# Performance work log

Measured on AMD Instinct MI355X. Metric: run time of the kernel, lower is better.

The kernel has to match this reference:

```python
import jax, jax.numpy as jnp
import numpy as np

D = 64
LENGTHS = (1, 32, 512)          # static BFS level sizes (traversal precomputed)
N_NODES = sum(LENGTHS)          # 545
BATCH = 2
NUM_PASSES = 2


def _lin_init(key, fan_in, fan_out):
    k1, k2 = jax.random.split(key)
    w = jax.random.normal(k1, (fan_out, fan_in), jnp.float32) / np.sqrt(fan_in)
    b = jax.random.normal(k2, (fan_out,), jnp.float32) * 0.01
    return w, b


def setup_inputs() -> dict:
    key = jax.random.key(0)
    ks = jax.random.split(key, 8)
    x = jax.random.normal(ks[0], (BATCH, N_NODES, D), jnp.float32)
    # tree edges consistent with LENGTHS (BFS levels, round-robin parent assignment)
    edges = []
    start_prev, start = 0, LENGTHS[0]
    for t, c in zip(LENGTHS, LENGTHS[1:]):
        for k in range(c):
            edges.append((start_prev + (k % t), start + k))
        start_prev = start
        start += c
    e = np.asarray(edges, dtype=np.int64).T  # [2, N-1]
    edge_index = jnp.broadcast_to(jnp.asarray(e)[None], (BATCH, 2, N_NODES - 1))
    w_ta, b_ta = _lin_init(ks[1], 2 * D, D)
    w_ca, b_ca = _lin_init(ks[2], 2 * D, D)
    w_tb, b_tb = _lin_init(ks[3], 2 * D, D)
    w_cb, b_cb = _lin_init(ks[4], 2 * D, D)
    w_u, b_u = _lin_init(ks[5], 2 * D, D)
    w_o, b_o = _lin_init(ks[6], 2 * D, D)
    w_mix = jax.random.normal(ks[7], (D, 1), jnp.float32)
    return {"x": x, "edge_index": edge_index,
            "w_ta": w_ta, "b_ta": b_ta, "w_ca": w_ca, "b_ca": b_ca,
            "w_tb": w_tb, "b_tb": b_tb, "w_cb": w_cb, "b_cb": b_cb,
            "w_mix": w_mix, "w_u": w_u, "b_u": b_u, "w_o": w_o, "b_o": b_o}


def reference(x, edge_index, w_ta, b_ta, w_ca, b_ca, w_tb, b_tb, w_cb, b_cb,
              w_mix, w_u, b_u, w_o, b_o):
    d = x.shape[-1]

    def gate_linear(w, b, main, s):
        # Linear(cat([main_col, s_k])) for every main column and every child k.
        # main: [d, m], s: [d, c] -> [c, d, m]
        return ((w[:, :d] @ main)[None, :, :]
                + (w[:, d:] @ s).T[:, :, None]
                + b[None, :, None])

    def prop(h, lengths):
        # h: [d, N]; update buffer accumulates across level pairs (as in source)
        update = jnp.zeros_like(h)
        offset = 0
        for t, c in zip(lengths, lengths[1:]):
            i, j = offset + t, offset + t + c
            T = h[:, offset:i]     # parent level  [d, t]
            C = h[:, i:j]          # child level   [d, c]
            Nb = h[:, offset:j]    # neighbors     [d, t+c]
            # softmax mix gate A, scaled by learned per-feature weight w_mix
            logits_a = jnp.concatenate(
                [gate_linear(w_ta, b_ta, T, C), gate_linear(w_ca, b_ca, C, C)], axis=-1)
            A = jax.nn.softmax(logits_a, axis=-1) * w_mix[None]   # [c, d, t+c]
            # softsign mix gate B
            pre_b = jnp.concatenate(
                [gate_linear(w_tb, b_tb, T, C), gate_linear(w_cb, b_cb, C, C)], axis=-1)
            Bm = pre_b / (1.0 + jnp.abs(pre_b))                   # [c, d, t+c]
            m = jnp.einsum('kdn,dn->kd', A + Bm, Nb)              # [c, d]
            s = C.T                                               # [c, d]
            u = jax.nn.sigmoid(m @ w_u[:, :d].T + s @ w_u[:, d:].T + b_u)
            o = jax.nn.relu(m @ w_o[:, :d].T + s @ w_o[:, d:].T + b_o)
            update = update.at[:, i:j].set((u * o + (1.0 - u) * m - s).T)
            h = h + update
            offset += t
        return h

    def per_graph(xg):  # xg: [N, d], already in BFS traversal order (perm = I)
        h = xg.T
        for _ in range(NUM_PASSES):
            h = prop(h, LENGTHS)
            h = prop(h, LENGTHS[::-1])
        return h.T

    return jax.vmap(per_graph)(x)
```

## Files before the change

### kernel.cpp

```cpp
#include <hip/hip_runtime.h>

#define D 64
#define NNODES 545
#define SNAPN 544
#define CN  64
#define CNP 32
#define NSL 4
#define NMS 8

__global__ void k_init(const float* __restrict__ x,
                       const float* __restrict__ w_ta, const float* __restrict__ w_ca,
                       const float* __restrict__ w_tb, const float* __restrict__ w_cb,
                       const float* __restrict__ w_u,  const float* __restrict__ w_o,
                       float* __restrict__ H, float* __restrict__ wT)
{
    int idx = blockIdx.x * 256 + threadIdx.x;
    const int NH = 2 * NNODES * D;
    if (idx < NH) { H[idx] = x[idx]; return; }
    int j = idx - NH;
    if (j >= 12 * 4096) return;
    int mat = j >> 12;
    int r   = j & 4095;
    int e   = r >> 6;
    int dd  = r & 63;
    const float* src;
    switch (mat >> 1) {
        case 0: src = w_ta; break;
        case 1: src = w_ca; break;
        case 2: src = w_tb; break;
        case 3: src = w_cb; break;
        case 4: src = w_u;  break;
        default: src = w_o; break;
    }
    int half = mat & 1;
    wT[j] = src[dd * 128 + half * 64 + e];
}

__global__ void k_stage(const float* __restrict__ H,
                        const float* __restrict__ wT,
                        float* __restrict__ snap,
                        float* __restrict__ Pb,
                        float* __restrict__ stT,
                        float* __restrict__ stC,
                        int off, int t, int c)
{
    __shared__ float Hs[4][64];
    __shared__ float PaS[4][64];
    int b = blockIdx.y;
    int tilesT = (t + 3) >> 2;
    int tile = blockIdx.x;
    int ln = threadIdx.x >> 6;
    int d  = threadIdx.x & 63;
    int regionC = (tile >= tilesT) ? 1 : 0;
    int tl = regionC ? (tile - tilesT) : tile;
    int n0 = tl * 4;
    int cnt = regionC ? c : t;
    int nodeBase = off + (regionC ? t : 0);
    int valid = (n0 + ln) < cnt;
    const float* Hb = H + b * NNODES * D;

    Hs[ln][d] = valid ? Hb[(nodeBase + n0 + ln) * D + d] : 0.0f;
    __syncthreads();

    const float* wA = wT + (regionC ? 2 * 4096 : 0);
    const float* wB = wT + (regionC ? 6 * 4096 : 4 * 4096);
    float acc_a = 0.0f, acc_b = 0.0f;
#pragma unroll 8
    for (int e = 0; e < 64; e++) {
        float h = Hs[ln][e];
        acc_a = fmaf(wA[e * 64 + d], h, acc_a);
        acc_b = fmaf(wB[e * 64 + d], h, acc_b);
    }
    int gn = (regionC ? t : 0) + n0 + ln;
    float* snapB = snap + b * SNAPN * D;
    float* PbB   = Pb   + b * SNAPN * D;
    if (valid) {
        PbB[gn * D + d]   = acc_b;
        snapB[gn * D + d] = Hs[ln][d];
    }
    PaS[ln][d] = valid ? acc_a : -3.0e38f;
    __syncthreads();

    if (threadIdx.x < 64) {
        int dd = threadIdx.x;
        float mx = -3.0e38f;
#pragma unroll
        for (int l = 0; l < 4; l++) mx = fmaxf(mx, PaS[l][dd]);
        int lim = cnt - n0; if (lim > 4) lim = 4;
        float se = 0.0f, sw = 0.0f;
        for (int l = 0; l < lim; l++) {
            float ev = expf(PaS[l][dd] - mx);
            se += ev;
            sw += ev * Hs[l][dd];
        }
        float* st = (regionC ? stC : stT) + b * 3 * 128 * 64;
        st[0 * 8192 + tl * 64 + dd] = mx;
        st[1 * 8192 + tl * 64 + dd] = se;
        st[2 * 8192 + tl * 64 + dd] = sw;
    }
}

__global__ void k_merge(const float* __restrict__ stT,
                        const float* __restrict__ stC,
                        float* __restrict__ stFin,
                        int t, int c)
{
    int r = blockIdx.x;
    int b = blockIdx.y;
    int d = threadIdx.x;
    const float* st = (r ? stC : stT) + b * 3 * 8192;
    int cnt = r ? c : t;
    int ntl = (cnt + 3) >> 2;
    float m = -3.0e38f, se = 0.0f, sw = 0.0f;
    for (int tl = 0; tl < ntl; tl++) {
        float m1 = st[tl * 64 + d];
        float s1 = st[8192 + tl * 64 + d];
        float w1 = st[2 * 8192 + tl * 64 + d];
        float nm = fmaxf(m, m1);
        float f0 = expf(m - nm), f1 = expf(m1 - nm);
        se = se * f0 + s1 * f1;
        sw = sw * f0 + w1 * f1;
        m  = nm;
    }
    float* o = stFin + (b * 2 + r) * 192;
    o[d] = m; o[64 + d] = se; o[128 + d] = sw;
}

__global__ void k_part(const float* __restrict__ wT,
                       const float* __restrict__ snap,
                       const float* __restrict__ Pb,
                       const float* __restrict__ b_tb, const float* __restrict__ b_cb,
                       const float* __restrict__ stT, const float* __restrict__ stC,
                       float* __restrict__ stMid,
                       float* __restrict__ accW,
                       int off, int t, int c)
{
    __shared__ float PS[CNP][D];
    __shared__ float SS[CNP][D];
    int kblk = gridDim.x - 4;
    int b  = blockIdx.z;

    if (blockIdx.x >= kblk) {
        if (threadIdx.x < 64) {
            int e = blockIdx.x - kblk;
            int r = e >> 1;
            int s = (e & 1) * 4 + blockIdx.y;
            int d = threadIdx.x;
            const float* st = (r ? stC : stT) + b * 3 * 8192;
            int cnt = r ? c : t;
            int ntl = (cnt + 3) >> 2;
            int tl0 = s * 16, tl1 = tl0 + 16; if (tl1 > ntl) tl1 = ntl;
            float m = -3.0e38f, se = 0.0f, sw = 0.0f;
            for (int tl = tl0; tl < tl1; tl++) {
                float m1 = st[tl * 64 + d];
                float s1 = st[8192 + tl * 64 + d];
                float w1 = st[2 * 8192 + tl * 64 + d];
                float nm = fmaxf(m, m1);
                float f0 = expf(m - nm), f1 = expf(m1 - nm);
                se = se * f0 + s1 * f1;
                sw = sw * f0 + w1 * f1;
                m  = nm;
            }
            float* o = stMid + ((b * 2 + r) * NMS + s) * 192;
            o[d] = m; o[64 + d] = se; o[128 + d] = sw;
        }
        return;
    }

    int s  = blockIdx.y;
    int kl = threadIdx.x >> 6;
    int d  = threadIdx.x & 63;
    int k  = blockIdx.x * 4 + kl;
    int valid = (k < c) ? 1 : 0;
    int kk = valid ? k : 0;
    const float* snapB = snap + b * SNAPN * D;
    const float* PbB   = Pb   + b * SNAPN * D;

    float offTb = b_tb[d], offCb = b_cb[d];
    const float* tbR = wT + 5 * 4096;
    const float* cbR = wT + 7 * 4096;
    const float* cptr = snapB + (t + kk) * 64;
#pragma unroll 8
    for (int e = 0; e < 64; e++) {
        float cv = cptr[e];
        offTb = fmaf(tbR[e * 64 + d], cv, offTb);
        offCb = fmaf(cbR[e * 64 + d], cv, offCb);
    }

    int NTOT = t + c;
    int nch = (NTOT + CNP - 1) / CNP;
    int cps = (nch + NSL - 1) / NSL;
    int ch0 = s * cps, ch1 = ch0 + cps; if (ch1 > nch) ch1 = nch;
    float acc = 0.0f;
    for (int ch = ch0; ch < ch1; ch++) {
        int n0 = ch * CNP;
        int cnt = NTOT - n0; if (cnt > CNP) cnt = CNP;
        __syncthreads();
        int tot4 = cnt * (D / 4);
        const float4* gp = (const float4*)(PbB   + n0 * D);
        const float4* gs = (const float4*)(snapB + n0 * D);
        float4* lp = (float4*)&PS[0][0];
        float4* ls = (float4*)&SS[0][0];
        for (int idx4 = threadIdx.x; idx4 < tot4; idx4 += 256) {
            lp[idx4] = gp[idx4];
            ls[idx4] = gs[idx4];
        }
        __syncthreads();
#pragma unroll 8
        for (int n = 0; n < cnt; n++) {
            int gn = n0 + n;
            float p = PS[n][d] + ((gn < t) ? offTb : offCb);
            float f = p / (1.0f + fabsf(p));
            acc = fmaf(f, SS[n][d], acc);
        }
    }
    accW[((s * 2 + b) * 512 + k) * 64 + d] = acc;
}

__global__ void k_fin(float* __restrict__ H,
                      const float* __restrict__ wT,
                      const float* __restrict__ snap,
                      const float* __restrict__ stMid,
                      const float* __restrict__ b_ta, const float* __restrict__ b_ca,
                      const float* __restrict__ w_mix,
                      const float* __restrict__ b_u, const float* __restrict__ b_o,
                      const float* __restrict__ accW,
                      float* __restrict__ updWS,
                      int off, int t, int c, int storeUpd, int reapply, int prev_i)
{
    __shared__ float mS[4][64];
    __shared__ float sS[4][64];
    int b  = blockIdx.y;
    int kl = threadIdx.x >> 6;
    int d  = threadIdx.x & 63;
    int k  = blockIdx.x * 4 + kl;
    int valid = (k < c) ? 1 : 0;
    int i = off + t;
    const float* snapB = snap + b * SNAPN * D;

    float mT = -3.0e38f, seT = 0.0f, swT = 0.0f;
    {
        const float* base = stMid + (b * 2 + 0) * NMS * 192;
#pragma unroll
        for (int s = 0; s < NMS; s++) {
            const float* p = base + s * 192;
            float m1 = p[d], s1 = p[64 + d], w1 = p[128 + d];
            float nm = fmaxf(mT, m1);
            float f0 = expf(mT - nm), f1 = expf(m1 - nm);
            seT = seT * f0 + s1 * f1;
            swT = swT * f0 + w1 * f1;
            mT = nm;
        }
    }
    float mC = -3.0e38f, seC = 0.0f, swC = 0.0f;
    {
        const float* base = stMid + (b * 2 + 1) * NMS * 192;
#pragma unroll
        for (int s = 0; s < NMS; s++) {
            const float* p = base + s * 192;
            float m1 = p[d], s1 = p[64 + d], w1 = p[128 + d];
            float nm = fmaxf(mC, m1);
            float f0 = expf(mC - nm), f1 = expf(m1 - nm);
            seC = seC * f0 + s1 * f1;
            swC = swC * f0 + w1 * f1;
            mC = nm;
        }
    }

    float offTa = b_ta[d], offCa = b_ca[d];
    const float* taR = wT + 1 * 4096;
    const float* caR = wT + 3 * 4096;
    int kk = valid ? k : 0;
    const float* cptr = snapB + (t + kk) * 64;
#pragma unroll 8
    for (int e = 0; e < 64; e++) {
        float cv = cptr[e];
        offTa = fmaf(taR[e * 64 + d], cv, offTa);
        offCa = fmaf(caR[e * 64 + d], cv, offCa);
    }

    float aT = mT + offTa, aC = mC + offCa;
    float M  = fmaxf(aT, aC);
    float eT = expf(aT - M), eC = expf(aC - M);
    float denom = eT * seT + eC * seC;
    float Apart = w_mix[d] * (eT * swT + eC * swC) / denom;

    float acc = 0.0f;
#pragma unroll
    for (int s = 0; s < NSL; s++) acc += accW[((s * 2 + b) * 512 + k) * 64 + d];
    float mval = Apart + acc;

    mS[kl][d] = mval;
    sS[kl][d] = snapB[(t + kk) * 64 + d];
    __syncthreads();

    const float* uL = wT + 8 * 4096;
    const float* uR = wT + 9 * 4096;
    const float* oL = wT + 10 * 4096;
    const float* oR = wT + 11 * 4096;
    float zU = b_u[d], zO = b_o[d];
#pragma unroll 8
    for (int e = 0; e < 64; e++) {
        float mv = mS[kl][e], sv = sS[kl][e];
        zU = fmaf(mv, uL[e * 64 + d], zU);
        zU = fmaf(sv, uR[e * 64 + d], zU);
        zO = fmaf(mv, oL[e * 64 + d], zO);
        zO = fmaf(sv, oR[e * 64 + d], zO);
    }
    float u  = 1.0f / (1.0f + expf(-zU));
    float o  = fmaxf(zO, 0.0f);
    float mm = mS[kl][d];
    float sv = sS[kl][d];
    float upd = u * o + (1.0f - u) * mm - sv;

    float* Hb = H + b * NNODES * D;
    if (valid) {
        Hb[(i + k) * D + d] += upd;
        if (storeUpd) updWS[b * 2048 + k * 64 + d] = upd;
    }
    if (reapply && blockIdx.x == 0) {
#pragma unroll
        for (int r = 0; r < 8; r++) {
            int idx = threadIdx.x + 256 * r;
            Hb[(prev_i + (idx >> 6)) * D + (idx & 63)] += updWS[b * 2048 + idx];
        }
    }
}

__global__ void k_gate(float* __restrict__ H,
                       const float* __restrict__ wT,
                       const float* __restrict__ snap,
                       const float* __restrict__ Pb,
                       const float* __restrict__ stFin,
                       const float* __restrict__ b_ta, const float* __restrict__ b_ca,
                       const float* __restrict__ b_tb, const float* __restrict__ b_cb,
                       const float* __restrict__ w_mix,
                       const float* __restrict__ b_u, const float* __restrict__ b_o,
                       float* __restrict__ updWS,
                       int off, int t, int c, int storeUpd, int reapply, int prev_i)
{
    __shared__ float PS[CN][D];
    __shared__ float SS[CN][D];
    __shared__ float mS[4][64];
    __shared__ float sS[4][64];
    int b  = blockIdx.y;
    int kl = threadIdx.x >> 6;
    int d  = threadIdx.x & 63;
    int k  = blockIdx.x * 4 + kl;
    int valid = (k < c) ? 1 : 0;
    int i = off + t;
    const float* snapB = snap + b * SNAPN * D;
    const float* PbB   = Pb   + b * SNAPN * D;

    const float* fB = stFin + b * 384;
    float mT = fB[d],       seT = fB[64 + d],  swT = fB[128 + d];
    float mC = fB[192 + d], seC = fB[256 + d], swC = fB[320 + d];

    float offTa = b_ta[d], offCa = b_ca[d], offTb = b_tb[d], offCb = b_cb[d];
    const float* taR = wT + 1 * 4096;
    const float* caR = wT + 3 * 4096;
    const float* tbR = wT + 5 * 4096;
    const float* cbR = wT + 7 * 4096;
    int kk = valid ? k : 0;
    const float* cptr = snapB + (t + kk) * 64;
#pragma unroll 8
    for (int e = 0; e < 64; e++) {
        float cv = cptr[e];
        offTa = fmaf(taR[e * 64 + d], cv, offTa);
        offCa = fmaf(caR[e * 64 + d], cv, offCa);
        offTb = fmaf(tbR[e * 64 + d], cv, offTb);
        offCb = fmaf(cbR[e * 64 + d], cv, offCb);
    }

    float aT = mT + offTa, aC = mC + offCa;
    float M  = fmaxf(aT, aC);
    float eT = expf(aT - M), eC = expf(aC - M);
    float denom = eT * seT + eC * seC;
    float Apart = w_mix[d] * (eT * swT + eC * swC) / denom;

    float acc = 0.0f;
    int NTOT = t + c;
    for (int n0 = 0; n0 < NTOT; n0 += CN) {
        int cnt = NTOT - n0; if (cnt > CN) cnt = CN;
        __syncthreads();
        int tot4 = cnt * (D / 4);
        const float4* gp = (const float4*)(PbB   + n0 * D);
        const float4* gs = (const float4*)(snapB + n0 * D);
        float4* lp = (float4*)&PS[0][0];
        float4* ls = (float4*)&SS[0][0];
        for (int idx4 = threadIdx.x; idx4 < tot4; idx4 += 256) {
            lp[idx4] = gp[idx4];
            ls[idx4] = gs[idx4];
        }
        __syncthreads();
#pragma unroll 8
        for (int n = 0; n < cnt; n++) {
            int gn = n0 + n;
            float p = PS[n][d] + ((gn < t) ? offTb : offCb);
            float f = p / (1.0f + fabsf(p));
            acc = fmaf(f, SS[n][d], acc);
        }
    }
    float mval = Apart + acc;

    mS[kl][d] = mval;
    sS[kl][d] = snapB[(t + kk) * 64 + d];
    __syncthreads();

    const float* uL = wT + 8 * 4096;
    const float* uR = wT + 9 * 4096;
    const float* oL = wT + 10 * 4096;
    const float* oR = wT + 11 * 4096;
    float zU = b_u[d], zO = b_o[d];
#pragma unroll 8
    for (int e = 0; e < 64; e++) {
        float mv = mS[kl][e], sv = sS[kl][e];
        zU = fmaf(mv, uL[e * 64 + d], zU);
        zU = fmaf(sv, uR[e * 64 + d], zU);
        zO = fmaf(mv, oL[e * 64 + d], zO);
        zO = fmaf(sv, oR[e * 64 + d], zO);
    }
    float u  = 1.0f / (1.0f + expf(-zU));
    float o  = fmaxf(zO, 0.0f);
    float mm = mS[kl][d];
    float sv = sS[kl][d];
    float upd = u * o + (1.0f - u) * mm - sv;

    float* Hb = H + b * NNODES * D;
    if (valid) {
        Hb[(i + k) * D + d] += upd;
        if (storeUpd) updWS[b * 2048 + k * 64 + d] = upd;
    }
    if (reapply && blockIdx.x == 0) {
#pragma unroll
        for (int r = 0; r < 8; r++) {
            int idx = threadIdx.x + 256 * r;
            Hb[(prev_i + (idx >> 6)) * D + (idx & 63)] += updWS[b * 2048 + idx];
        }
    }
}

extern "C" void kernel_launch(void* const* d_in, const int* in_sizes, int n_in,
                              void* d_out, int out_size, void* d_ws, size_t ws_size,
                              hipStream_t stream) {
    const float* x    = (const float*)d_in[0];
    const float* w_ta = (const float*)d_in[2];
    const float* b_ta = (const float*)d_in[3];
    const float* w_ca = (const float*)d_in[4];
    const float* b_ca = (const float*)d_in[5];
    const float* w_tb = (const float*)d_in[6];
    const float* b_tb = (const float*)d_in[7];
    const float* w_cb = (const float*)d_in[8];
    const float* b_cb = (const float*)d_in[9];
    const float* w_mix= (const float*)d_in[10];
    const float* w_u  = (const float*)d_in[11];
    const float* b_u  = (const float*)d_in[12];
    const float* w_o  = (const float*)d_in[13];
    const float* b_o  = (const float*)d_in[14];

    float* H  = (float*)d_out;
    float* ws = (float*)d_ws;
    float* wT    = ws;
    float* snap  = wT + 49152;
    float* Pb    = snap + 69632;
    float* stT   = Pb + 69632;
    float* stC   = stT + 49152;
    float* upd   = stC + 49152;
    float* stFin = upd + 4096;
    float* accW  = stFin + 768;
    float* stMid = accW + 262144;

    const size_t NEEDED = (size_t)(49152 + 69632 + 69632 + 49152 + 49152 + 4096 + 768
                                   + (size_t)NSL * 2 * 512 * 64 + 2 * 2 * NMS * 192) * 4;
    int useSplit = (ws_size >= NEEDED) ? 1 : 0;

    {
        int total = 2 * NNODES * D + 12 * 4096;
        k_init<<<dim3((total + 255) / 256), 256, 0, stream>>>(
            x, w_ta, w_ca, w_tb, w_cb, w_u, w_o, H, wT);
    }

    struct St { int off, t, c, store, reapply, prev_i; };
    const St steps[4] = {
        {0,   1,  32, 1, 0, 0},
        {1,  32, 512, 0, 1, 1},
        {0, 512,  32, 1, 0, 0},
        {512, 32,  1, 0, 1, 512},
    };
    for (int p = 0; p < 2; p++) {
        for (int s = 0; s < 4; s++) {
            St st = steps[s];
            int tilesT = (st.t + 3) / 4, tilesC = (st.c + 3) / 4;
            k_stage<<<dim3(tilesT + tilesC, 2), 256, 0, stream>>>(
                H, wT, snap, Pb, stT, stC, st.off, st.t, st.c);
            int kblk = (st.c + 3) / 4;
            if (useSplit) {
                k_part<<<dim3(kblk + 4, NSL, 2), 256, 0, stream>>>(
                    wT, snap, Pb, b_tb, b_cb, stT, stC, stMid, accW,
                    st.off, st.t, st.c);
                k_fin<<<dim3(kblk, 2), 256, 0, stream>>>(
                    H, wT, snap, stMid, b_ta, b_ca, w_mix, b_u, b_o, accW, upd,
                    st.off, st.t, st.c, st.store, st.reapply, st.prev_i);
            } else {
                k_merge<<<dim3(2, 2), 64, 0, stream>>>(
                    stT, stC, stFin, st.t, st.c);
                k_gate<<<dim3(kblk, 2), 256, 0, stream>>>(
                    H, wT, snap, Pb, stFin,
                    b_ta, b_ca, b_tb, b_cb, w_mix, b_u, b_o, upd,
                    st.off, st.t, st.c, st.store, st.reapply, st.prev_i);
            }
        }
    }
}
```

Measured before the change: 220.7 us.

## Fuse tiny-level gate steps into one kernel and widen split-K for large levels

Adds a fused k_gate4 kernel for levels where t+c <= 64. It merges the softmax stats, gate offsets, the softsign accumulation and the update in one launch, removing the separate k_part/k_fin launches for those steps. For the larger levels the split count rises from 4 to 8, and the k_part inner loop reads Pb/snap straight from global memory instead of staging through shared memory with barriers. This trades launch count and barrier overhead for more partial-sum traffic in accW and uncached global reads.

```diff
diff --git a/kernel.cpp b/kernel.cpp
--- a/kernel.cpp
+++ b/kernel.cpp
@@ -5,7 +5,7 @@
 #define SNAPN 544
 #define CN  64
 #define CNP 32
-#define NSL 4
+#define NSLMAX 16
 #define NMS 8
 
 __global__ void k_init(const float* __restrict__ x,
@@ -126,6 +126,141 @@
     o[d] = m; o[64 + d] = se; o[128 + d] = sw;
 }
 
+__global__ void k_gate4(float* __restrict__ H,
+                        const float* __restrict__ wT,
+                        const float* __restrict__ snap,
+                        const float* __restrict__ Pb,
+                        const float* __restrict__ stT,
+                        const float* __restrict__ stC,
+                        const float* __restrict__ b_ta, const float* __restrict__ b_ca,
+                        const float* __restrict__ b_tb, const float* __restrict__ b_cb,
+                        const float* __restrict__ w_mix,
+                        const float* __restrict__ b_u, const float* __restrict__ b_o,
+                        float* __restrict__ updWS,
+                        int off, int t, int c, int storeUpd, int reapply, int prev_i)
+{
+    __shared__ float PS[CN][D];
+    __shared__ float SS[CN][D];
+    __shared__ float mS[4][64];
+    __shared__ float sS[4][64];
+    int b  = blockIdx.y;
+    int kl = threadIdx.x >> 6;
+    int d  = threadIdx.x & 63;
+    int k  = blockIdx.x * 4 + kl;
+    int valid = (k < c) ? 1 : 0;
+    int i = off + t;
+    const float* snapB = snap + b * SNAPN * D;
+    const float* PbB   = Pb   + b * SNAPN * D;
+
+    int nT = (t + 3) >> 2, nC = (c + 3) >> 2;
+    const float* sT = stT + b * 3 * 8192;
+    float mT = -3.0e38f, seT = 0.0f, swT = 0.0f;
+    for (int tl = 0; tl < nT; tl++) {
+        float m1 = sT[tl * 64 + d];
+        float s1 = sT[8192 + tl * 64 + d];
+        float w1 = sT[2 * 8192 + tl * 64 + d];
+        float nm = fmaxf(mT, m1);
+        float f0 = expf(mT - nm), f1 = expf(m1 - nm);
+        seT = seT * f0 + s1 * f1;
+        swT = swT * f0 + w1 * f1;
+        mT = nm;
+    }
+    const float* sC = stC + b * 3 * 8192;
+    float mC = -3.0e38f, seC = 0.0f, swC = 0.0f;
+    for (int tl = 0; tl < nC; tl++) {
+        float m1 = sC[tl * 64 + d];
+        float s1 = sC[8192 + tl * 64 + d];
+        float w1 = sC[2 * 8192 + tl * 64 + d];
+        float nm = fmaxf(mC, m1);
+        float f0 = expf(mC - nm), f1 = expf(m1 - nm);
+        seC = seC * f0 + s1 * f1;
+        swC = swC * f0 + w1 * f1;
+        mC = nm;
+    }
+
+    float offTa = b_ta[d], offCa = b_ca[d], offTb = b_tb[d], offCb = b_cb[d];
+    const float* taR = wT + 1 * 4096;
+    const float* caR = wT + 3 * 4096;
+    const float* tbR = wT + 5 * 4096;
+    const float* cbR = wT + 7 * 4096;
+    int kk = valid ? k : 0;
+    const float* cptr = snapB + (t + kk) * 64;
+#pragma unroll 4
+    for (int e = 0; e < 64; e++) {
+        float cv = cptr[e];
+        offTa = fmaf(taR[e * 64 + d], cv, offTa);
+        offCa = fmaf(caR[e * 64 + d], cv, offCa);
+        offTb = fmaf(tbR[e * 64 + d], cv, offTb);
+        offCb = fmaf(cbR[e * 64 + d], cv, offCb);
+    }
+
+    float aT = mT + offTa, aC = mC + offCa;
+    float M  = fmaxf(aT, aC);
+    float eT = expf(aT - M), eC = expf(aC - M);
+    float denom = eT * seT + eC * seC;
+    float Apart = w_mix[d] * (eT * swT + eC * swC) / denom;
+
+    float acc = 0.0f;
+    int NTOT = t + c;
+    for (int n0 = 0; n0 < NTOT; n0 += CN) {
+        int cnt = NTOT - n0; if (cnt > CN) cnt = CN;
+        __syncthreads();
+        int tot4 = cnt * (D / 4);
+        const float4* gp = (const float4*)(PbB   + n0 * D);
+        const float4* gs = (const float4*)(snapB + n0 * D);
+        float4* lp = (float4*)&PS[0][0];
+        float4* ls = (float4*)&SS[0][0];
+        for (int idx4 = threadIdx.x; idx4 < tot4; idx4 += 256) {
+            lp[idx4] = gp[idx4];
+            ls[idx4] = gs[idx4];
+        }
+        __syncthreads();
+        for (int n = 0; n < cnt; n++) {
+            int gn = n0 + n;
+            float p = PS[n][d] + ((gn < t) ? offTb : offCb);
+            float f = p / (1.0f + fabsf(p));
+            acc = fmaf(f, SS[n][d], acc);
+        }
+    }
+    float mval = Apart + acc;
+
+    mS[kl][d] = mval;
+    sS[kl][d] = snapB[(t + kk) * 64 + d];
+    __syncthreads();
+
+    const float* uL = wT + 8 * 4096;
+    const float* uR = wT + 9 * 4096;
+    const float* oL = wT + 10 * 4096;
+    const float* oR = wT + 11 * 4096;
+    float zU = b_u[d], zO = b_o[d];
+#pragma unroll 4
+    for (int e = 0; e < 64; e++) {
+        float mv = mS[kl][e], sv = sS[kl][e];
+        zU = fmaf(mv, uL[e * 64 + d], zU);
+        zU = fmaf(sv, uR[e * 64 + d], zU);
+        zO = fmaf(mv, oL[e * 64 + d], zO);
+        zO = fmaf(sv, oR[e * 64 + d], zO);
+    }
+    float u  = 1.0f / (1.0f + expf(-zU));
+    float o  = fmaxf(zO, 0.0f);
+    float mm = mS[kl][d];
+    float sv = sS[kl][d];
+    float upd = u * o + (1.0f - u) * mm - sv;
+
+    float* Hb = H + b * NNODES * D;
+    if (valid) {
+        Hb[(i + k) * D + d] += upd;
+        if (storeUpd) updWS[b * 2048 + k * 64 + d] = upd;
+    }
+    if (reapply && blockIdx.x == 0) {
+#pragma unroll
+        for (int r = 0; r < 8; r++) {
+            int idx = threadIdx.x + 256 * r;
+            Hb[(prev_i + (idx >> 6)) * D + (idx & 63)] += updWS[b * 2048 + idx];
+        }
+    }
+}
+
 __global__ void k_part(const float* __restrict__ wT,
                        const float* __restrict__ snap,
                        const float* __restrict__ Pb,
@@ -133,15 +268,13 @@
                        const float* __restrict__ stT, const float* __restrict__ stC,
                        float* __restrict__ stMid,
                        float* __restrict__ accW,
-                       int off, int t, int c)
+                       int off, int t, int c, int nsl)
 {
-    __shared__ float PS[CNP][D];
-    __shared__ float SS[CNP][D];
     int kblk = gridDim.x - 4;
     int b  = blockIdx.z;
 
     if (blockIdx.x >= kblk) {
-        if (threadIdx.x < 64) {
+        if (blockIdx.y < 4 && threadIdx.x < 64) {
             int e = blockIdx.x - kblk;
             int r = e >> 1;
             int s = (e & 1) * 4 + blockIdx.y;
@@ -189,30 +322,17 @@
 
     int NTOT = t + c;
     int nch = (NTOT + CNP - 1) / CNP;
-    int cps = (nch + NSL - 1) / NSL;
-    int ch0 = s * cps, ch1 = ch0 + cps; if (ch1 > nch) ch1 = nch;
+    int cps = (nch + nsl - 1) / nsl;
+    int nlo = s * cps * CNP;
+    int nhi = (s + 1) * cps * CNP; if (nhi > NTOT) nhi = NTOT;
     float acc = 0.0f;
-    for (int ch = ch0; ch < ch1; ch++) {
-        int n0 = ch * CNP;
-        int cnt = NTOT - n0; if (cnt > CNP) cnt = CNP;
-        __syncthreads();
-        int tot4 = cnt * (D / 4);
-        const float4* gp = (const float4*)(PbB   + n0 * D);
-        const float4* gs = (const float4*)(snapB + n0 * D);
-        float4* lp = (float4*)&PS[0][0];
-        float4* ls = (float4*)&SS[0][0];
-        for (int idx4 = threadIdx.x; idx4 < tot4; idx4 += 256) {
-            lp[idx4] = gp[idx4];
-            ls[idx4] = gs[idx4];
-        }
-        __syncthreads();
-#pragma unroll 8
-        for (int n = 0; n < cnt; n++) {
-            int gn = n0 + n;
-            float p = PS[n][d] + ((gn < t) ? offTb : offCb);
-            float f = p / (1.0f + fabsf(p));
-            acc = fmaf(f, SS[n][d], acc);
-        }
+#pragma unroll 8
+    for (int n = nlo; n < nhi; n++) {
+        float pb = PbB[n * 64 + d];
+        float sv = snapB[n * 64 + d];
+        float p = pb + ((n < t) ? offTb : offCb);
+        float f = p / (1.0f + fabsf(p));
+        acc = fmaf(f, sv, acc);
     }
     accW[((s * 2 + b) * 512 + k) * 64 + d] = acc;
 }
@@ -226,7 +346,8 @@
                       const float* __restrict__ b_u, const float* __restrict__ b_o,
                       const float* __restrict__ accW,
                       float* __restrict__ updWS,
-                      int off, int t, int c, int storeUpd, int reapply, int prev_i)
+                      int off, int t, int c, int storeUpd, int reapply, int prev_i,
+                      int nsl)
 {
     __shared__ float mS[4][64];
     __shared__ float sS[4][64];
@@ -286,8 +407,8 @@
     float Apart = w_mix[d] * (eT * swT + eC * swC) / denom;
 
     float acc = 0.0f;
-#pragma unroll
-    for (int s = 0; s < NSL; s++) acc += accW[((s * 2 + b) * 512 + k) * 64 + d];
+#pragma unroll 4
+    for (int s = 0; s < nsl; s++) acc += accW[((s * 2 + b) * 512 + k) * 64 + d];
     float mval = Apart + acc;
 
     mS[kl][d] = mval;
@@ -468,10 +589,10 @@
     float* upd   = stC + 49152;
     float* stFin = upd + 4096;
     float* accW  = stFin + 768;
-    float* stMid = accW + 262144;
+    float* stMid = accW + 1048576;
 
     const size_t NEEDED = (size_t)(49152 + 69632 + 69632 + 49152 + 49152 + 4096 + 768
-                                   + (size_t)NSL * 2 * 512 * 64 + 2 * 2 * NMS * 192) * 4;
+                                   + (size_t)NSLMAX * 2 * 512 * 64 + 2 * 2 * NMS * 192) * 4;
     int useSplit = (ws_size >= NEEDED) ? 1 : 0;
 
     {
@@ -494,20 +615,27 @@
             k_stage<<<dim3(tilesT + tilesC, 2), 256, 0, stream>>>(
                 H, wT, snap, Pb, stT, stC, st.off, st.t, st.c);
             int kblk = (st.c + 3) / 4;
-            if (useSplit) {
-                k_part<<<dim3(kblk + 4, NSL, 2), 256, 0, stream>>>(
-                    wT, snap, Pb, b_tb, b_cb, stT, stC, stMid, accW,
-                    st.off, st.t, st.c);
-                k_fin<<<dim3(kblk, 2), 256, 0, stream>>>(
-                    H, wT, snap, stMid, b_ta, b_ca, w_mix, b_u, b_o, accW, upd,
-                    st.off, st.t, st.c, st.store, st.reapply, st.prev_i);
-            } else {
+            int tiny = (st.t + st.c) <= 64;
+            if (!useSplit) {
                 k_merge<<<dim3(2, 2), 64, 0, stream>>>(
                     stT, stC, stFin, st.t, st.c);
                 k_gate<<<dim3(kblk, 2), 256, 0, stream>>>(
                     H, wT, snap, Pb, stFin,
                     b_ta, b_ca, b_tb, b_cb, w_mix, b_u, b_o, upd,
                     st.off, st.t, st.c, st.store, st.reapply, st.prev_i);
+            } else if (tiny) {
+                k_gate4<<<dim3(kblk, 2), 256, 0, stream>>>(
+                    H, wT, snap, Pb, stT, stC,
+                    b_ta, b_ca, b_tb, b_cb, w_mix, b_u, b_o, upd,
+                    st.off, st.t, st.c, st.store, st.reapply, st.prev_i);
+            } else {
+                const int nsl = 8;
+                k_part<<<dim3(kblk + 4, nsl, 2), 256, 0, stream>>>(
+                    wT, snap, Pb, b_tb, b_cb, stT, stC, stMid, accW,
+                    st.off, st.t, st.c, nsl);
+                k_fin<<<dim3(kblk, 2), 256, 0, stream>>>(
+                    H, wT, snap, stMid, b_ta, b_ca, w_mix, b_u, b_o, accW, upd,
+                    st.off, st.t, st.c, st.store, st.reapply, st.prev_i, nsl);
             }
         }
     }
```

After: 225.9 us. 2.3% more time.
